# Kernel tuning notes

Measured on AMD Instinct MI355X. Metric: run time of the kernel, lower is better.

## Reference

```python
import jax, jax.numpy as jnp
import numpy as np

G = 7          # 7x7 feature map -> 49 nodes per image
N = G * G
K = 3          # knn_k
NEG_SLOPE = 0.2  # PyG GATConv default leaky_relu slope


def build_spatial_edges():
    # 8-neighborhood grid edges on the 7x7 map, directed (src -> dst)
    src, dst = [], []
    for r in range(G):
        for c in range(G):
            i = r * G + c
            for dr in (-1, 0, 1):
                for dc in (-1, 0, 1):
                    if dr == 0 and dc == 0:
                        continue
                    rr, cc = r + dr, c + dc
                    if 0 <= rr < G and 0 <= cc < G:
                        src.append(rr * G + cc)
                        dst.append(i)
    return np.array([src, dst], dtype=np.int32)

SPATIAL = build_spatial_edges()  # [2, 312]


def build_edges(x):
    """x: [B, N, F] node features -> (src, dst) each [B, E].
    Edges = spatial 8-neighborhood + feature-space kNN (k=3) + self-loops."""
    B = x.shape[0]
    sq = jnp.sum(x * x, axis=-1)                               # [B, N]
    d = sq[:, :, None] + sq[:, None, :] - 2.0 * jnp.einsum('bnf,bmf->bnm', x, x)
    d = d + jnp.eye(N, dtype=x.dtype) * 1e9                    # exclude self
    _, nbr = jax.lax.top_k(-d, K)                              # [B, N, K]
    knn_src = nbr.reshape(B, N * K)
    knn_dst = jnp.broadcast_to(jnp.repeat(jnp.arange(N, dtype=jnp.int32), K)[None], (B, N * K))
    sp = jnp.asarray(SPATIAL)
    Es = sp.shape[1]
    loops = jnp.arange(N, dtype=jnp.int32)
    src = jnp.concatenate([jnp.broadcast_to(sp[0][None], (B, Es)), knn_src.astype(jnp.int32),
                           jnp.broadcast_to(loops[None], (B, N))], axis=1)
    dst = jnp.concatenate([jnp.broadcast_to(sp[1][None], (B, Es)), knn_dst,
                           jnp.broadcast_to(loops[None], (B, N))], axis=1)
    return src, dst


def gat_layer(x, src, dst, W, a_src, a_dst, b, concat):
    """PyG-style GATConv (eval mode, no dropout). x: [N,F], src/dst: [E]."""
    H, C = a_src.shape
    h = (x @ W).reshape(N, H, C)                               # [N, H, C]
    es = jnp.sum(h * a_src[None], axis=-1)                     # [N, H]
    ed = jnp.sum(h * a_dst[None], axis=-1)                     # [N, H]
    e = jax.nn.leaky_relu(es[src] + ed[dst], NEG_SLOPE)        # [E, H]
    m = jax.ops.segment_max(e, dst, num_segments=N)            # [N, H]
    m = jnp.where(jnp.isfinite(m), m, 0.0)
    p = jnp.exp(e - m[dst])
    denom = jax.ops.segment_sum(p, dst, num_segments=N)
    alpha = p / jnp.maximum(denom[dst], 1e-16)                 # softmax over incoming edges
    out = jax.ops.segment_sum(alpha[:, :, None] * h[src], dst, num_segments=N)  # [N, H, C]
    out = out.reshape(N, H * C) if concat else out.mean(axis=1)
    return out + b


def setup_inputs() -> dict:
    key = jax.random.key(0)
    ks = jax.random.split(key, 14)
    B, F, Hd, Cd, O, NC = 256, 1024, 8, 128, 256, 14
    s = 0.05
    return {
        'feat_map': jax.random.normal(ks[0], (B, F, G, G), dtype=jnp.float32),
        'W1': jax.random.normal(ks[1], (F, Hd * Cd), dtype=jnp.float32) * s,
        'a_src1': jax.random.normal(ks[2], (Hd, Cd), dtype=jnp.float32) * s,
        'a_dst1': jax.random.normal(ks[3], (Hd, Cd), dtype=jnp.float32) * s,
        'b1': jnp.zeros((Hd * Cd,), dtype=jnp.float32),
        'W2': jax.random.normal(ks[4], (Hd * Cd, O), dtype=jnp.float32) * s,
        'a_src2': jax.random.normal(ks[5], (1, O), dtype=jnp.float32) * s,
        'a_dst2': jax.random.normal(ks[6], (1, O), dtype=jnp.float32) * s,
        'b2': jnp.zeros((O,), dtype=jnp.float32),
        'Wc1': jax.random.normal(ks[7], (O, O), dtype=jnp.float32) * s,
        'bc1': jnp.zeros((O,), dtype=jnp.float32),
        'Wc2': jax.random.normal(ks[8], (O, NC), dtype=jnp.float32) * s,
        'bc2': jnp.zeros((NC,), dtype=jnp.float32),
    }


def reference(feat_map, W1, a_src1, a_dst1, b1, W2, a_src2, a_dst2, b2, Wc1, bc1, Wc2, bc2):
    B = feat_map.shape[0]
    # backbone output relu + flatten 7x7 map into 49 nodes
    x = jax.nn.relu(feat_map).reshape(B, -1, N).transpose(0, 2, 1)  # [B, N, 1024]
    src, dst = build_edges(x)

    def per_graph(xg, sg, dg):
        h = jax.nn.elu(gat_layer(xg, sg, dg, W1, a_src1, a_dst1, b1, True))
        h = jax.nn.elu(gat_layer(h, sg, dg, W2, a_src2, a_dst2, b2, False))
        return h.mean(axis=0)                                   # global mean pool -> [256]

    pooled = jax.vmap(per_graph)(x, src, dst)                   # [B, 256]
    return jax.nn.relu(pooled @ Wc1 + bc1) @ Wc2 + bc2          # [B, 14]
```

## Files before the change

kernel.cpp:

```cpp
#include <hip/hip_runtime.h>

#define GDIM 7
#define NN 49
#define FDIM 1024
#define HD 8
#define CD 128
#define ODIM 256
#define NC 14
#define MAXE 12

typedef __attribute__((ext_vector_type(4))) float f32x4;
typedef __attribute__((ext_vector_type(8))) short s16x8;

struct us4 { unsigned short x, y, z, w; };

__device__ __forceinline__ unsigned short f2bf(float x) {
  unsigned u = __float_as_uint(x);
  return (unsigned short)((u + 0x7fffu + ((u >> 16) & 1u)) >> 16);
}
__device__ __forceinline__ float bf2f(unsigned short h) {
  return __uint_as_float((unsigned)h << 16);
}

#define GLOAD_LDS16(g, l)                                          \
  __builtin_amdgcn_global_load_lds(                                \
      (const __attribute__((address_space(1))) void*)(g),          \
      (__attribute__((address_space(3))) void*)(l), 16, 0, 0)

__global__ void __launch_bounds__(256) relu_transpose_kernel(
    const float* __restrict__ F, float* __restrict__ X,
    unsigned short* __restrict__ Xh, unsigned short* __restrict__ Xl) {
  const int b  = blockIdx.x >> 4;
  const int f0 = (blockIdx.x & 15) << 6;
  const int tid = threadIdx.x;
  __shared__ float lds[64 * NN];
  const float* src = F + (size_t)b * FDIM * NN + (size_t)f0 * NN;
  for (int idx = tid; idx < 64 * NN; idx += 256) lds[idx] = src[idx];
  __syncthreads();
  for (int pass = 0; pass < 13; pass++) {
    int n = pass * 4 + (tid >> 6);
    int fi = tid & 63;
    if (n < NN) {
      float v = lds[fi * NN + n];
      v = v > 0.f ? v : 0.f;
      size_t o = ((size_t)b * NN + n) * FDIM + f0 + fi;
      X[o] = v;
      unsigned short h = f2bf(v);
      Xh[o] = h;
      Xl[o] = f2bf(v - bf2f(h));
    }
  }
}

__global__ void __launch_bounds__(256) knn_kernel(
    const float* __restrict__ X, int* __restrict__ knn) {
  const int b = blockIdx.x, tid = threadIdx.x;
  __shared__ float xs[56][68];
  __shared__ float gram[56][57];
  const float* Xb = X + (size_t)b * NN * FDIM;

  const int tr = tid / 14, tc = tid % 14;
  float acc[4][4];
#pragma unroll
  for (int i = 0; i < 4; i++)
#pragma unroll
    for (int j = 0; j < 4; j++) acc[i][j] = 0.f;

  for (int c0 = 0; c0 < FDIM; c0 += 64) {
    __syncthreads();
    for (int idx = tid; idx < NN * 16; idx += 256) {
      int n = idx >> 4, q = idx & 15;
      *(float4*)&xs[n][q << 2] =
          *(const float4*)&Xb[(size_t)n * FDIM + c0 + (q << 2)];
    }
    __syncthreads();
    if (tid < 196) {
#pragma unroll
      for (int k4 = 0; k4 < 64; k4 += 4) {
        float4 a[4], bb[4];
#pragma unroll
        for (int i = 0; i < 4; i++) a[i]  = *(const float4*)&xs[tr + 14 * i][k4];
#pragma unroll
        for (int j = 0; j < 4; j++) bb[j] = *(const float4*)&xs[tc + 14 * j][k4];
#pragma unroll
        for (int i = 0; i < 4; i++)
#pragma unroll
          for (int j = 0; j < 4; j++)
            acc[i][j] += a[i].x * bb[j].x + a[i].y * bb[j].y +
                         a[i].z * bb[j].z + a[i].w * bb[j].w;
      }
    }
  }
  if (tid < 196) {
#pragma unroll
    for (int i = 0; i < 4; i++)
#pragma unroll
      for (int j = 0; j < 4; j++) gram[tr + 14 * i][tc + 14 * j] = acc[i][j];
  }
  __syncthreads();
  if (tid < NN) {
    const int n = tid;
    const float sqn = gram[n][n];
    float d0 = 1e30f, d1 = 1e30f, d2 = 1e30f;
    int i0 = 0, i1 = 0, i2 = 0;
    for (int m = 0; m < NN; m++) {
      if (m == n) continue;
      float d = sqn + gram[m][m] - 2.f * gram[n][m];
      if (d < d0)      { d2=d1; i2=i1; d1=d0; i1=i0; d0=d; i0=m; }
      else if (d < d1) { d2=d1; i2=i1; d1=d;  i1=m; }
      else if (d < d2) { d2=d;  i2=m; }
    }
    knn[((size_t)b * NN + n) * 3 + 0] = i0;
    knn[((size_t)b * NN + n) * 3 + 1] = i1;
    knn[((size_t)b * NN + n) * 3 + 2] = i2;
  }
}

__global__ void __launch_bounds__(256) wconvT_kernel(
    const float* __restrict__ W, int K, int N,
    unsigned short* __restrict__ WhT, unsigned short* __restrict__ WlT) {
  __shared__ float t[64][65];
  const int nbx = N >> 6;
  const int bx = blockIdx.x % nbx, by = blockIdx.x / nbx;
  const int r0 = by << 6, c0 = bx << 6;
  const int tid = threadIdx.x;
#pragma unroll
  for (int i = 0; i < 16; i++) {
    int r = i * 4 + (tid >> 6), c = tid & 63;
    t[r][c] = W[(size_t)(r0 + r) * N + c0 + c];
  }
  __syncthreads();
#pragma unroll
  for (int i = 0; i < 16; i++) {
    int n = i * 4 + (tid >> 6);
    int k = tid & 63;
    float x = t[k][n];
    unsigned short h = f2bf(x);
    size_t o = (size_t)(c0 + n) * K + r0 + k;
    WhT[o] = h;
    WlT[o] = f2bf(x - bf2f(h));
  }
}

__global__ void __launch_bounds__(256) gemm_bf16x3(
    const unsigned short* __restrict__ A_h, const unsigned short* __restrict__ A_l,
    const unsigned short* __restrict__ BT_h, const unsigned short* __restrict__ BT_l,
    float* __restrict__ C, int M, int N, int K) {
  __shared__ unsigned short sAh[128][32], sAl[128][32];
  __shared__ unsigned short sBh[128][32], sBl[128][32];
  const int tid = threadIdx.x;
  const int w = tid >> 6, lane = tid & 63;
  const int nbx = N >> 7;
  const int bx = blockIdx.x % nbx, by = blockIdx.x / nbx;
  const int row0 = by << 7, col0 = bx << 7;
  const int wr = (w >> 1) << 6, wc = (w & 1) << 6;
  const int srow = lane >> 2, schk = lane & 3;
  const int fr = lane & 15, fk = (lane >> 4) << 3;

  f32x4 acc[4][4];
#pragma unroll
  for (int m = 0; m < 4; m++)
#pragma unroll
    for (int n = 0; n < 4; n++) acc[m][n] = (f32x4){0.f, 0.f, 0.f, 0.f};

  for (int k0 = 0; k0 < K; k0 += 32) {
    __syncthreads();
#pragma unroll
    for (int i = 0; i < 2; i++) {
      const int rbase = (w << 5) + (i << 4);
      const int gr = rbase + srow;
      const size_t ga = (size_t)(row0 + gr) * K + k0 + (schk << 3);
      GLOAD_LDS16(A_h + ga, &sAh[rbase][0]);
      GLOAD_LDS16(A_l + ga, &sAl[rbase][0]);
      const size_t gb = (size_t)(col0 + gr) * K + k0 + (schk << 3);
      GLOAD_LDS16(BT_h + gb, &sBh[rbase][0]);
      GLOAD_LDS16(BT_l + gb, &sBl[rbase][0]);
    }
    __syncthreads();
    s16x8 ah[4], al[4], bh[4], bl[4];
#pragma unroll
    for (int m = 0; m < 4; m++) {
      ah[m] = *(const s16x8*)&sAh[wr + (m << 4) + fr][fk];
      al[m] = *(const s16x8*)&sAl[wr + (m << 4) + fr][fk];
      bh[m] = *(const s16x8*)&sBh[wc + (m << 4) + fr][fk];
      bl[m] = *(const s16x8*)&sBl[wc + (m << 4) + fr][fk];
    }
#pragma unroll
    for (int m = 0; m < 4; m++)
#pragma unroll
      for (int n = 0; n < 4; n++) {
        acc[m][n] = __builtin_amdgcn_mfma_f32_16x16x32_bf16(ah[m], bh[n], acc[m][n], 0, 0, 0);
        acc[m][n] = __builtin_amdgcn_mfma_f32_16x16x32_bf16(ah[m], bl[n], acc[m][n], 0, 0, 0);
        acc[m][n] = __builtin_amdgcn_mfma_f32_16x16x32_bf16(al[m], bh[n], acc[m][n], 0, 0, 0);
      }
  }
  const int crow = (lane >> 4) << 2, ccol = lane & 15;
#pragma unroll
  for (int m = 0; m < 4; m++)
#pragma unroll
    for (int n = 0; n < 4; n++)
#pragma unroll
      for (int v = 0; v < 4; v++)
        C[(size_t)(row0 + wr + (m << 4) + crow + v) * N + col0 + wc + (n << 4) + ccol] =
            acc[m][n][v];
}

__global__ void __launch_bounds__(256) attn1_prep(
    const float* __restrict__ H, const int* __restrict__ knn,
    const float* __restrict__ a_src, const float* __restrict__ a_dst,
    int* __restrict__ srcs_g, int* __restrict__ cnt_g,
    float* __restrict__ alpha_g) {
  const int b = blockIdx.x, tid = threadIdx.x;
  __shared__ float es[NN][HD], ed[NN][HD];
  __shared__ int srcs[NN][MAXE];
  __shared__ int cnt[NN];
  const float* Hb = H + (size_t)b * NN * FDIM;

  for (int p = tid; p < NN * HD; p += 256) {
    int n = p >> 3, h = p & 7;
    const float* hr = Hb + (size_t)n * FDIM + h * CD;
    float s1 = 0.f, s2 = 0.f;
    for (int c = 0; c < CD; c += 4) {
      float4 hv = *(const float4*)&hr[c];
      float4 as = *(const float4*)&a_src[h * CD + c];
      float4 ad = *(const float4*)&a_dst[h * CD + c];
      s1 += hv.x*as.x + hv.y*as.y + hv.z*as.z + hv.w*as.w;
      s2 += hv.x*ad.x + hv.y*ad.y + hv.z*ad.z + hv.w*ad.w;
    }
    es[n][h] = s1; ed[n][h] = s2;
  }
  if (tid < NN) {
    int i = tid, r = i / GDIM, c = i % GDIM, k = 0;
    for (int dr = -1; dr <= 1; dr++)
      for (int dc = -1; dc <= 1; dc++) {
        if (dr == 0 && dc == 0) continue;
        int rr = r + dr, cc = c + dc;
        if (rr >= 0 && rr < GDIM && cc >= 0 && cc < GDIM)
          srcs[i][k++] = rr * GDIM + cc;
      }
    srcs[i][k++] = knn[((size_t)b * NN + i) * 3 + 0];
    srcs[i][k++] = knn[((size_t)b * NN + i) * 3 + 1];
    srcs[i][k++] = knn[((size_t)b * NN + i) * 3 + 2];
    srcs[i][k++] = i;
    cnt[i] = k;
    cnt_g[(size_t)b * NN + i] = k;
    for (int j = 0; j < MAXE; j++)
      srcs_g[((size_t)b * NN + i) * MAXE + j] = srcs[i][j < k ? j : 0];
  }
  __syncthreads();
  for (int p = tid; p < NN * HD; p += 256) {
    int i = p >> 3, h = p & 7;
    int k = cnt[i];
    float e[MAXE];
    float m = -1e30f;
#pragma unroll
    for (int j = 0; j < MAXE; j++) {
      if (j < k) {
        float v = es[srcs[i][j]][h] + ed[i][h];
        v = v >= 0.f ? v : 0.2f * v;
        e[j] = v;
        m = fmaxf(m, v);
      }
    }
    float denom = 0.f;
#pragma unroll
    for (int j = 0; j < MAXE; j++) {
      if (j < k) { e[j] = expf(e[j] - m); denom += e[j]; }
    }
    float inv = 1.f / fmaxf(denom, 1e-16f);
#pragma unroll
    for (int j = 0; j < MAXE; j++) {
      if (j < k)
        alpha_g[(((size_t)b * NN + i) * MAXE + j) * HD + h] = e[j] * inv;
    }
  }
}

__global__ void __launch_bounds__(256) attn1_agg(
    const float* __restrict__ H, const int* __restrict__ srcs_g,
    const int* __restrict__ cnt_g, const float* __restrict__ alpha_g,
    const float* __restrict__ b1,
    unsigned short* __restrict__ Zh, unsigned short* __restrict__ Zl) {
  const int bid = blockIdx.x;
  const int b = bid / NN;
  const int tid = threadIdx.x;
  __shared__ float al[MAXE][HD];
  __shared__ int ss[MAXE];
  const int k = cnt_g[bid];
  if (tid < MAXE * HD) al[tid >> 3][tid & 7] = alpha_g[(size_t)bid * MAXE * HD + tid];
  if (tid < MAXE) ss[tid] = srcs_g[(size_t)bid * MAXE + tid];
  __syncthreads();
  const float4* Hb = (const float4*)(H + (size_t)b * NN * FDIM);
  const int h = tid >> 5;
  float4 acc = ((const float4*)b1)[tid];
  for (int j = 0; j < k; j++) {
    float a = al[j][h];
    float4 v = Hb[(size_t)ss[j] * (FDIM / 4) + tid];
    acc.x += a * v.x; acc.y += a * v.y; acc.z += a * v.z; acc.w += a * v.w;
  }
  acc.x = acc.x > 0.f ? acc.x : expm1f(acc.x);
  acc.y = acc.y > 0.f ? acc.y : expm1f(acc.y);
  acc.z = acc.z > 0.f ? acc.z : expm1f(acc.z);
  acc.w = acc.w > 0.f ? acc.w : expm1f(acc.w);
  us4 hv, lv;
  hv.x = f2bf(acc.x); lv.x = f2bf(acc.x - bf2f(hv.x));
  hv.y = f2bf(acc.y); lv.y = f2bf(acc.y - bf2f(hv.y));
  hv.z = f2bf(acc.z); lv.z = f2bf(acc.z - bf2f(hv.z));
  hv.w = f2bf(acc.w); lv.w = f2bf(acc.w - bf2f(hv.w));
  *(us4*)&Zh[(size_t)bid * FDIM + (tid << 2)] = hv;
  *(us4*)&Zl[(size_t)bid * FDIM + (tid << 2)] = lv;
}

__global__ void __launch_bounds__(256) attn2_prep(
    const float* __restrict__ H2, const int* __restrict__ srcs_g,
    const int* __restrict__ cnt_g, const float* __restrict__ a_src,
    const float* __restrict__ a_dst, float* __restrict__ alpha_g) {
  const int b = blockIdx.x, tid = threadIdx.x;
  __shared__ float es[NN], ed[NN];
  const float* Hb = H2 + (size_t)b * NN * ODIM;
  if (tid < NN) {
    const float* hr = Hb + (size_t)tid * ODIM;
    float s1 = 0.f, s2 = 0.f;
    for (int c = 0; c < ODIM; c += 4) {
      float4 hv = *(const float4*)&hr[c];
      float4 as = *(const float4*)&a_src[c];
      float4 ad = *(const float4*)&a_dst[c];
      s1 += hv.x*as.x + hv.y*as.y + hv.z*as.z + hv.w*as.w;
      s2 += hv.x*ad.x + hv.y*ad.y + hv.z*ad.z + hv.w*ad.w;
    }
    es[tid] = s1; ed[tid] = s2;
  }
  __syncthreads();
  if (tid < NN) {
    const int i = tid;
    const int k = cnt_g[(size_t)b * NN + i];
    float e[MAXE];
    float m = -1e30f;
#pragma unroll
    for (int j = 0; j < MAXE; j++) {
      if (j < k) {
        int s = srcs_g[((size_t)b * NN + i) * MAXE + j];
        float v = es[s] + ed[i];
        v = v >= 0.f ? v : 0.2f * v;
        e[j] = v;
        m = fmaxf(m, v);
      }
    }
    float denom = 0.f;
#pragma unroll
    for (int j = 0; j < MAXE; j++) {
      if (j < k) { e[j] = expf(e[j] - m); denom += e[j]; }
    }
    float inv = 1.f / fmaxf(denom, 1e-16f);
#pragma unroll
    for (int j = 0; j < MAXE; j++) {
      if (j < k) alpha_g[((size_t)b * NN + i) * MAXE + j] = e[j] * inv;
    }
  }
}

__global__ void __launch_bounds__(256) attn2_agg(
    const float* __restrict__ H2, const int* __restrict__ srcs_g,
    const int* __restrict__ cnt_g, const float* __restrict__ alpha_g,
    const float* __restrict__ b2, float* __restrict__ Z2) {
  const int bid = blockIdx.x;
  const int b = bid / NN;
  const int tid = threadIdx.x;
  __shared__ float al[MAXE];
  __shared__ int ss[MAXE];
  const int k = cnt_g[bid];
  if (tid < MAXE) {
    al[tid] = alpha_g[(size_t)bid * MAXE + tid];
    ss[tid] = srcs_g[(size_t)bid * MAXE + tid];
  }
  __syncthreads();
  const float* Hb = H2 + (size_t)b * NN * ODIM;
  float acc = b2[tid];
  for (int j = 0; j < k; j++)
    acc += al[j] * Hb[(size_t)ss[j] * ODIM + tid];
  acc = acc > 0.f ? acc : expm1f(acc);
  Z2[(size_t)bid * ODIM + tid] = acc;
}

__global__ void __launch_bounds__(256) pool_kernel(
    const float* __restrict__ Z2, float* __restrict__ pooled) {
  const int b = blockIdx.x, c = threadIdx.x;
  float s = 0.f;
  for (int i = 0; i < NN; i++)
    s += Z2[((size_t)b * NN + i) * ODIM + c];
  pooled[(size_t)b * ODIM + c] = s * (1.f / 49.f);
}

__global__ void __launch_bounds__(256) classifier_kernel(
    const float* __restrict__ pooled, const float* __restrict__ Wc1,
    const float* __restrict__ bc1, const float* __restrict__ Wc2,
    const float* __restrict__ bc2, float* __restrict__ out) {
  const int b = blockIdx.x, tid = threadIdx.x;
  __shared__ float p[ODIM];
  __shared__ float t[ODIM];
  p[tid] = pooled[(size_t)b * ODIM + tid];
  __syncthreads();
  float a = bc1[tid];
  for (int c = 0; c < ODIM; c++) a += p[c] * Wc1[(size_t)c * ODIM + tid];
  t[tid] = a > 0.f ? a : 0.f;
  __syncthreads();
  if (tid < NC) {
    float o = bc2[tid];
    for (int j = 0; j < ODIM; j++) o += t[j] * Wc2[(size_t)j * NC + tid];
    out[(size_t)b * NC + tid] = o;
  }
}

extern "C" void kernel_launch(void* const* d_in, const int* in_sizes, int n_in,
                              void* d_out, int out_size, void* d_ws, size_t ws_size,
                              hipStream_t stream) {
  const float* feat   = (const float*)d_in[0];
  const float* W1     = (const float*)d_in[1];
  const float* a_src1 = (const float*)d_in[2];
  const float* a_dst1 = (const float*)d_in[3];
  const float* b1     = (const float*)d_in[4];
  const float* W2     = (const float*)d_in[5];
  const float* a_src2 = (const float*)d_in[6];
  const float* a_dst2 = (const float*)d_in[7];
  const float* b2     = (const float*)d_in[8];
  const float* Wc1    = (const float*)d_in[9];
  const float* bc1    = (const float*)d_in[10];
  const float* Wc2    = (const float*)d_in[11];
  const float* bc2    = (const float*)d_in[12];

  const int B = in_sizes[0] / (FDIM * NN);
  const int M = B * NN;

  const size_t xE = (size_t)M * FDIM;
  float* X  = (float*)d_ws;
  float* H1 = X + xE;
  unsigned short* Xh = (unsigned short*)(H1 + xE);
  unsigned short* Xl = Xh + xE;
  unsigned short* W1hT = Xl + xE;
  unsigned short* W1lT = W1hT + (size_t)FDIM * FDIM;
  unsigned short* W2hT = W1lT + (size_t)FDIM * FDIM;
  unsigned short* W2lT = W2hT + (size_t)ODIM * FDIM;
  int*   knn    = (int*)(W2lT + (size_t)ODIM * FDIM);
  int*   srcs_g = knn + (size_t)M * 3;
  int*   cnt_g  = srcs_g + (size_t)M * MAXE;
  float* alpha1 = (float*)(cnt_g + M);
  float* alpha2 = alpha1 + (size_t)M * MAXE * HD;
  float* pooled = alpha2 + (size_t)M * MAXE;
  float* H2  = X;
  float* Z2  = H1;
  unsigned short* Z1h = Xh;
  unsigned short* Z1l = Xl;

  relu_transpose_kernel<<<B * 16, 256, 0, stream>>>(feat, X, Xh, Xl);
  knn_kernel<<<B, 256, 0, stream>>>(X, knn);
  wconvT_kernel<<<(FDIM / 64) * (FDIM / 64), 256, 0, stream>>>(W1, FDIM, FDIM, W1hT, W1lT);
  wconvT_kernel<<<(FDIM / 64) * (ODIM / 64), 256, 0, stream>>>(W2, FDIM, ODIM, W2hT, W2lT);
  gemm_bf16x3<<<(M / 128) * (FDIM / 128), 256, 0, stream>>>(
      Xh, Xl, W1hT, W1lT, H1, M, FDIM, FDIM);
  attn1_prep<<<B, 256, 0, stream>>>(H1, knn, a_src1, a_dst1, srcs_g, cnt_g, alpha1);
  attn1_agg<<<M, 256, 0, stream>>>(H1, srcs_g, cnt_g, alpha1, b1, Z1h, Z1l);
  gemm_bf16x3<<<(M / 128) * (ODIM / 128), 256, 0, stream>>>(
      Z1h, Z1l, W2hT, W2lT, H2, M, ODIM, FDIM);
  attn2_prep<<<B, 256, 0, stream>>>(H2, srcs_g, cnt_g, a_src2, a_dst2, alpha2);
  attn2_agg<<<M, 256, 0, stream>>>(H2, srcs_g, cnt_g, alpha2, b2, Z2);
  pool_kernel<<<B, 256, 0, stream>>>(Z2, pooled);
  classifier_kernel<<<B, 256, 0, stream>>>(pooled, Wc1, bc1, Wc2, bc2, (float*)d_out);
}
```

Baseline: 367.9 us.

## Double GEMM K-tile, XOR-swizzle LDS layout, and remap blocks across XCDs

The bf16x3 GEMM now stages a 64-wide K slice per iteration instead of 32, which halves the number of barrier pairs per K loop. LDS columns are XOR-swizzled by row so the fragment reads avoid bank conflicts, and the global-load addresses are permuted to match. Block IDs are remapped so consecutive output tiles land on the same XCD, aiming for better L2 reuse of shared A and B panels. LDS usage doubles to 64KB per block, which may reduce occupancy.

```diff
diff --git a/kernel.cpp b/kernel.cpp
--- a/kernel.cpp
+++ b/kernel.cpp
@@ -146,16 +146,23 @@
     const unsigned short* __restrict__ A_h, const unsigned short* __restrict__ A_l,
     const unsigned short* __restrict__ BT_h, const unsigned short* __restrict__ BT_l,
     float* __restrict__ C, int M, int N, int K) {
-  __shared__ unsigned short sAh[128][32], sAl[128][32];
-  __shared__ unsigned short sBh[128][32], sBl[128][32];
+  __shared__ unsigned short sAh[128][64], sAl[128][64];
+  __shared__ unsigned short sBh[128][64], sBl[128][64];
   const int tid = threadIdx.x;
   const int w = tid >> 6, lane = tid & 63;
   const int nbx = N >> 7;
-  const int bx = blockIdx.x % nbx, by = blockIdx.x / nbx;
+  const int nwg = gridDim.x;
+  const int q = nwg >> 3, r = nwg & 7;
+  const int xcd = blockIdx.x & 7, loc = blockIdx.x >> 3;
+  const int wg = (xcd < r) ? (xcd * (q + 1) + loc)
+                           : (r * (q + 1) + (xcd - r) * q + loc);
+  const int bx = wg % nbx, by = wg / nbx;
   const int row0 = by << 7, col0 = bx << 7;
   const int wr = (w >> 1) << 6, wc = (w & 1) << 6;
-  const int srow = lane >> 2, schk = lane & 3;
-  const int fr = lane & 15, fk = (lane >> 4) << 3;
+  const int sgr = lane >> 3;
+  const int schunk = lane & 7;
+  const int fr = lane & 15;
+  const int fq = lane >> 4;
 
   f32x4 acc[4][4];
 #pragma unroll
@@ -163,38 +170,47 @@
 #pragma unroll
     for (int n = 0; n < 4; n++) acc[m][n] = (f32x4){0.f, 0.f, 0.f, 0.f};
 
-  for (int k0 = 0; k0 < K; k0 += 32) {
+  for (int k0 = 0; k0 < K; k0 += 64) {
     __syncthreads();
 #pragma unroll
-    for (int i = 0; i < 2; i++) {
-      const int rbase = (w << 5) + (i << 4);
-      const int gr = rbase + srow;
-      const size_t ga = (size_t)(row0 + gr) * K + k0 + (schk << 3);
+    for (int i = 0; i < 4; i++) {
+      const int rbase = (w << 5) + (i << 3);
+      const int gr = rbase + sgr;
+      const int sc = schunk ^ (gr & 7);
+      const size_t ga = (size_t)(row0 + gr) * K + k0 + (sc << 3);
       GLOAD_LDS16(A_h + ga, &sAh[rbase][0]);
       GLOAD_LDS16(A_l + ga, &sAl[rbase][0]);
-      const size_t gb = (size_t)(col0 + gr) * K + k0 + (schk << 3);
+      const size_t gb = (size_t)(col0 + gr) * K + k0 + (sc << 3);
       GLOAD_LDS16(BT_h + gb, &sBh[rbase][0]);
       GLOAD_LDS16(BT_l + gb, &sBl[rbase][0]);
     }
     __syncthreads();
-    s16x8 ah[4], al[4], bh[4], bl[4];
-#pragma unroll
-    for (int m = 0; m < 4; m++) {
-      ah[m] = *(const s16x8*)&sAh[wr + (m << 4) + fr][fk];
-      al[m] = *(const s16x8*)&sAl[wr + (m << 4) + fr][fk];
-      bh[m] = *(const s16x8*)&sBh[wc + (m << 4) + fr][fk];
-      bl[m] = *(const s16x8*)&sBl[wc + (m << 4) + fr][fk];
-    }
-#pragma unroll
-    for (int m = 0; m < 4; m++)
-#pragma unroll
-      for (int n = 0; n < 4; n++) {
-        acc[m][n] = __builtin_amdgcn_mfma_f32_16x16x32_bf16(ah[m], bh[n], acc[m][n], 0, 0, 0);
-        acc[m][n] = __builtin_amdgcn_mfma_f32_16x16x32_bf16(ah[m], bl[n], acc[m][n], 0, 0, 0);
-        acc[m][n] = __builtin_amdgcn_mfma_f32_16x16x32_bf16(al[m], bh[n], acc[m][n], 0, 0, 0);
+#pragma unroll
+    for (int ks = 0; ks < 2; ks++) {
+      const int cb = (ks << 2) + fq;
+      s16x8 ah[4], al[4], bh[4], bl[4];
+#pragma unroll
+      for (int m = 0; m < 4; m++) {
+        const int ra = wr + (m << 4) + fr;
+        const int ca = (cb ^ (ra & 7)) << 3;
+        ah[m] = *(const s16x8*)&sAh[ra][ca];
+        al[m] = *(const s16x8*)&sAl[ra][ca];
+        const int rb = wc + (m << 4) + fr;
+        const int cbn = (cb ^ (rb & 7)) << 3;
+        bh[m] = *(const s16x8*)&sBh[rb][cbn];
+        bl[m] = *(const s16x8*)&sBl[rb][cbn];
       }
-  }
-  const int crow = (lane >> 4) << 2, ccol = lane & 15;
+#pragma unroll
+      for (int m = 0; m < 4; m++)
+#pragma unroll
+        for (int n = 0; n < 4; n++) {
+          acc[m][n] = __builtin_amdgcn_mfma_f32_16x16x32_bf16(ah[m], bh[n], acc[m][n], 0, 0, 0);
+          acc[m][n] = __builtin_amdgcn_mfma_f32_16x16x32_bf16(ah[m], bl[n], acc[m][n], 0, 0, 0);
+          acc[m][n] = __builtin_amdgcn_mfma_f32_16x16x32_bf16(al[m], bh[n], acc[m][n], 0, 0, 0);
+        }
+    }
+  }
+  const int crow = fq << 2, ccol = fr;
 #pragma unroll
   for (int m = 0; m < 4; m++)
 #pragma unroll
```

After: 325.2 us. -11.6%, faster.
